# Optimization experiments

Hardware: AMD Instinct MI355X
Metric: run time of the kernel (lower is better)

Reference implementation:

```python
import jax, jax.numpy as jnp
import numpy as np

N_NODES = 50000
N_EDGES = 800000
IN_F, H_F, OUT_F = 256, 256, 128


def setup_inputs() -> dict:
    key = jax.random.key(0)
    k1, k2, k3, k4, k5, k6 = jax.random.split(key, 6)
    in_feat = jax.random.normal(k1, (N_NODES, IN_F), dtype=jnp.float32)
    src = jax.random.randint(k2, (N_EDGES,), 0, N_NODES, dtype=jnp.int32)
    dst = jax.random.randint(k3, (N_EDGES,), 0, N_NODES, dtype=jnp.int32)
    s1 = 1.0 / np.sqrt(IN_F)
    s2 = 1.0 / np.sqrt(H_F)
    W1 = jax.random.uniform(k4, (IN_F, H_F), dtype=jnp.float32, minval=-s1, maxval=s1)
    b1 = jnp.zeros((H_F,), dtype=jnp.float32)
    W2 = jax.random.uniform(k5, (H_F, OUT_F), dtype=jnp.float32, minval=-s2, maxval=s2)
    b2 = jnp.zeros((OUT_F,), dtype=jnp.float32)
    return {"in_feat": in_feat, "src": src, "dst": dst,
            "W1": W1, "b1": b1, "W2": W2, "b2": b2}


def _graph_conv(x, W, b, src, dst, n_nodes):
    # DGL GraphConv with norm='both':
    #   h = D_in^{-1/2} A D_out^{-1/2} (X W) + b   (degrees clamped to min 1)
    ones = jnp.ones((src.shape[0],), dtype=x.dtype)
    deg_out = jax.ops.segment_sum(ones, src, num_segments=n_nodes)
    deg_in = jax.ops.segment_sum(ones, dst, num_segments=n_nodes)
    norm_out = jax.lax.rsqrt(jnp.maximum(deg_out, 1.0))  # [N]
    norm_in = jax.lax.rsqrt(jnp.maximum(deg_in, 1.0))    # [N]
    h = (x @ W) * norm_out[:, None]                       # [N, F_out]
    agg = jax.ops.segment_sum(h[src], dst, num_segments=n_nodes)  # SpMM
    return agg * norm_in[:, None] + b


def reference(in_feat, src, dst, W1, b1, W2, b2):
    n = in_feat.shape[0]
    h = _graph_conv(in_feat, W1, b1, src, dst, n)
    h = jax.nn.relu(h)
    h = _graph_conv(h, W2, b2, src, dst, n)
    # dgl.mean_nodes over a single graph -> mean across all nodes
    return jnp.mean(h, axis=0)  # [OUT_F]
```

## Files before the change

### kernel.cpp

```cpp
#include <hip/hip_runtime.h>


#define NNODES 50000
#define NEDGES 800000
#define G1_BM   ((NNODES + 127) / 128)
#define MEGA_NB 3911
#define WS_NB   4096

typedef __bf16 bf16x8 __attribute__((ext_vector_type(8)));
typedef float f32x4 __attribute__((ext_vector_type(4)));
typedef float f32x2 __attribute__((ext_vector_type(2)));

__device__ __forceinline__ unsigned short f2b(float f) {
    union { float f; unsigned u; } v; v.f = f;
    unsigned r = 0x7fffu + ((v.u >> 16) & 1u);
    return (unsigned short)((v.u + r) >> 16);
}
__device__ __forceinline__ unsigned char f2fp8(float x) {
    return (unsigned char)(__builtin_amdgcn_cvt_pk_fp8_f32(x, x, 0, false) & 0xff);
}
__device__ __forceinline__ float rdeg(int d) {
    return __frsqrt_rn((float)max(d, 1));
}

__global__ void k_cast_w1(const float* __restrict__ W1, unsigned short* __restrict__ W1t) {
    int id = blockIdx.x * blockDim.x + threadIdx.x;
    int k = id >> 8, n = id & 255;
    W1t[n * 256 + k] = f2b(W1[id]);
}

__global__ __launch_bounds__(256) void k_mega1(
    const int* __restrict__ src, const int* __restrict__ dst,
    int* __restrict__ degOut, int* __restrict__ degIn,
    unsigned short* __restrict__ col2, unsigned short* __restrict__ dst2,
    const float* __restrict__ X, const unsigned short* __restrict__ W1t,
    unsigned char* __restrict__ H, int M) {
    __shared__ __align__(16) unsigned short As[128][40];
    __shared__ __align__(16) unsigned short Bs[128][40];

    int bid = blockIdx.x;
    int tid = threadIdx.x;

    if ((bid % 5) != 4) {
        int did = bid - (bid + 1) / 5;
        int e = did * 256 + tid;
        if (e < NEDGES) {
            int s = src[e], d = dst[e];
            int si = atomicAdd(&degIn[d], 1);
            if (si < 64) col2[d * 64 + si] = (unsigned short)s;
            int so = atomicAdd(&degOut[s], 1);
            if (so < 64) dst2[s * 64 + so] = (unsigned short)d;
        }
        return;
    }

    int g = bid / 5;
    int bm = g % G1_BM, bn = g / G1_BM;
    int m0 = bm * 128, n0 = bn * 128;
    int lane = tid & 63, wave = tid >> 6;
    int wm = (wave >> 1) * 64, wn = (wave & 1) * 64;
    int q = lane >> 4, r16 = lane & 15;

    f32x4 acc[4][4];
#pragma unroll
    for (int i = 0; i < 4; i++)
#pragma unroll
        for (int j = 0; j < 4; j++) acc[i][j] = 0.f;

    int c0 = tid, c1 = tid + 256;
    int r0 = c0 >> 2, k0c = (c0 & 3) * 8;
    int r1 = c1 >> 2, k1c = (c1 & 3) * 8;
    const float* Ar0 = X + (size_t)min(m0 + r0, M - 1) * 256;
    const float* Ar1 = X + (size_t)min(m0 + r1, M - 1) * 256;
    const unsigned short* Br0 = W1t + (size_t)(n0 + r0) * 256;
    const unsigned short* Br1 = W1t + (size_t)(n0 + r1) * 256;

    auto pk2u = [](float a, float b) -> unsigned {
        unsigned short x = f2b(a), y = f2b(b);
        return (unsigned)x | ((unsigned)y << 16);
    };

    for (int k0 = 0; k0 < 256; k0 += 32) {
        float4 fa0 = *(const float4*)(Ar0 + k0 + k0c);
        float4 fa1 = *(const float4*)(Ar0 + k0 + k0c + 4);
        float4 fb0 = *(const float4*)(Ar1 + k0 + k1c);
        float4 fb1 = *(const float4*)(Ar1 + k0 + k1c + 4);
        uint4 vb0 = *(const uint4*)(Br0 + k0 + k0c);
        uint4 vb1 = *(const uint4*)(Br1 + k0 + k1c);
        uint4 va0 = make_uint4(pk2u(fa0.x, fa0.y), pk2u(fa0.z, fa0.w), pk2u(fa1.x, fa1.y), pk2u(fa1.z, fa1.w));
        uint4 va1 = make_uint4(pk2u(fb0.x, fb0.y), pk2u(fb0.z, fb0.w), pk2u(fb1.x, fb1.y), pk2u(fb1.z, fb1.w));
        __syncthreads();
        *(uint4*)&As[r0][k0c] = va0;
        *(uint4*)&As[r1][k1c] = va1;
        *(uint4*)&Bs[r0][k0c] = vb0;
        *(uint4*)&Bs[r1][k1c] = vb1;
        __syncthreads();
        bf16x8 af[4], bf[4];
#pragma unroll
        for (int i = 0; i < 4; i++)
            af[i] = *(const bf16x8*)&As[wm + i * 16 + r16][q * 8];
#pragma unroll
        for (int j = 0; j < 4; j++)
            bf[j] = *(const bf16x8*)&Bs[wn + j * 16 + r16][q * 8];
#pragma unroll
        for (int i = 0; i < 4; i++)
#pragma unroll
            for (int j = 0; j < 4; j++)
                acc[i][j] = __builtin_amdgcn_mfma_f32_16x16x32_bf16(af[i], bf[j], acc[i][j], 0, 0, 0);
    }

#pragma unroll
    for (int i = 0; i < 4; i++) {
#pragma unroll
        for (int rr = 0; rr < 4; rr++) {
            int m = m0 + wm + i * 16 + q * 4 + rr;
            if (m < M) {
                unsigned char* Hp = H + (size_t)m * 256 + n0 + wn + r16;
#pragma unroll
                for (int j = 0; j < 4; j++)
                    Hp[j * 16] = f2fp8(acc[i][j][rr]);
            }
        }
    }
}

__global__ __launch_bounds__(256) void k_spmm_wsum(
    const unsigned char* __restrict__ H, const int* __restrict__ degIn,
    const int* __restrict__ degOut, const unsigned short* __restrict__ col2,
    const unsigned short* __restrict__ dst2, const float* __restrict__ bias,
    float* __restrict__ vpart) {
    __shared__ float sm[4][256];
    int wave = threadIdx.x >> 6;
    int lane = threadIdx.x & 63;
    int f = lane * 4;
    const unsigned char* Hf = H + f;
    float4 bv = *(const float4*)(bias + f);
    float vac0 = 0.f, vac1 = 0.f, vac2 = 0.f, vac3 = 0.f;

    for (int qd = blockIdx.x; qd < NNODES / 4; qd += gridDim.x) {
        int node = qd * 4 + wave;

        int dO = min(degOut[node], 64);
        float sIn = 0.f;
        if (lane < dO) sIn = rdeg(degIn[(int)dst2[node * 64 + lane]]);
#pragma unroll
        for (int o = 32; o > 0; o >>= 1) sIn += __shfl_xor(sIn, o);
        float wn = rdeg(dO) * sIn;

        int s = node * 64;
        int e = s + min(degIn[node], 64);
        float a0 = 0.f, a1 = 0.f, a2 = 0.f, a3 = 0.f;
        int i = s;
        for (; i + 8 <= e; i += 8) {
            int c[8];
#pragma unroll
            for (int u = 0; u < 8; u++) c[u] = __builtin_amdgcn_readfirstlane((int)col2[i + u]);
            float w[8]; unsigned v[8];
#pragma unroll
            for (int u = 0; u < 8; u++) {
                w[u] = rdeg(degOut[c[u]]);
                v[u] = *(const unsigned*)(Hf + (size_t)c[u] * 256);
            }
#pragma unroll
            for (int u = 0; u < 8; u++) {
                f32x2 lo = __builtin_amdgcn_cvt_pk_f32_fp8(v[u], false);
                f32x2 hi = __builtin_amdgcn_cvt_pk_f32_fp8(v[u], true);
                a0 += lo.x * w[u]; a1 += lo.y * w[u];
                a2 += hi.x * w[u]; a3 += hi.y * w[u];
            }
        }
        for (; i < e; i++) {
            int c = __builtin_amdgcn_readfirstlane((int)col2[i]);
            float w = rdeg(degOut[c]);
            unsigned v = *(const unsigned*)(Hf + (size_t)c * 256);
            f32x2 lo = __builtin_amdgcn_cvt_pk_f32_fp8(v, false);
            f32x2 hi = __builtin_amdgcn_cvt_pk_f32_fp8(v, true);
            a0 += lo.x * w; a1 += lo.y * w;
            a2 += hi.x * w; a3 += hi.y * w;
        }
        float nm = rdeg(e - s);
        vac0 += wn * fmaxf(a0 * nm + bv.x, 0.f);
        vac1 += wn * fmaxf(a1 * nm + bv.y, 0.f);
        vac2 += wn * fmaxf(a2 * nm + bv.z, 0.f);
        vac3 += wn * fmaxf(a3 * nm + bv.w, 0.f);
    }

    *(float4*)&sm[wave][f] = make_float4(vac0, vac1, vac2, vac3);
    __syncthreads();
    int t = threadIdx.x;
    float s4 = sm[0][t] + sm[1][t] + sm[2][t] + sm[3][t];
    vpart[(size_t)blockIdx.x * 256 + t] = s4;
}

__global__ __launch_bounds__(256) void k_red1(const float* __restrict__ vpart,
                                              float* __restrict__ vred) {
    int b = blockIdx.x;
    int t = threadIdx.x;
    float s = 0.f;
    for (int i = b; i < WS_NB; i += 64) s += vpart[(size_t)i * 256 + t];
    vred[(size_t)b * 256 + t] = s;
}

__global__ __launch_bounds__(1024) void k_final(
    const float* __restrict__ vred, const float* __restrict__ W2,
    const float* __restrict__ b2, float* __restrict__ out) {
    __shared__ float part[4][256];
    __shared__ float v[256];
    int t = threadIdx.x;
    int feat = t & 255, pr = t >> 8;
    float s = 0.f;
    for (int i = pr; i < 64; i += 4) s += vred[(size_t)i * 256 + feat];
    part[pr][feat] = s;
    __syncthreads();
    if (t < 256) v[t] = part[0][t] + part[1][t] + part[2][t] + part[3][t];
    __syncthreads();
    if (t < 128) {
        float o = 0.f;
        for (int k = 0; k < 256; k++) o += v[k] * W2[k * 128 + t];
        out[t] = o * (1.0f / (float)NNODES) + b2[t];
    }
}

extern "C" void kernel_launch(void* const* d_in, const int* in_sizes, int n_in,
                              void* d_out, int out_size, void* d_ws, size_t ws_size,
                              hipStream_t stream) {
    const float* X   = (const float*)d_in[0];
    const int*   src = (const int*)d_in[1];
    const int*   dst = (const int*)d_in[2];
    const float* W1  = (const float*)d_in[3];
    const float* b1  = (const float*)d_in[4];
    const float* W2  = (const float*)d_in[5];
    const float* b2  = (const float*)d_in[6];
    float* out = (float*)d_out;

    const int n = NNODES;

    char* p = (char*)d_ws;
    auto carve = [&](size_t bytes) -> void* {
        void* r = (void*)p;
        p += (bytes + 255) & ~(size_t)255;
        return r;
    };
    int*   degOut  = (int*)carve((size_t)2 * n * sizeof(int));
    int*   degIn   = degOut + n;
    unsigned short* col2 = (unsigned short*)carve((size_t)n * 64 * 2);
    unsigned short* dst2 = (unsigned short*)carve((size_t)n * 64 * 2);
    unsigned short* W1t  = (unsigned short*)carve((size_t)256 * 256 * 2);
    unsigned char*  bufA = (unsigned char*)carve((size_t)n * 256);
    float* vpart  = (float*)carve((size_t)WS_NB * 256 * sizeof(float));
    float* vred   = (float*)carve((size_t)64 * 256 * sizeof(float));

    hipMemsetAsync(degOut, 0, (size_t)2 * n * sizeof(int), stream);

    k_cast_w1<<<256, 256, 0, stream>>>(W1, W1t);

    k_mega1<<<MEGA_NB, 256, 0, stream>>>(src, dst, degOut, degIn, col2, dst2, X, W1t, bufA, n);

    k_spmm_wsum<<<WS_NB, 256, 0, stream>>>(bufA, degIn, degOut, col2, dst2, b1, vpart);

    k_red1<<<64, 256, 0, stream>>>(vpart, vred);
    k_final<<<1, 1024, 0, stream>>>(vred, W2, b2, out);
}
```

Before: 246.6 us.

## Pre-scale GEMM output by out-degree norm in a separate pass before SpMM

The GEMM now writes bf16 output, and a new k_scale pass multiplies each row by its out-degree norm and packs it to fp8. This removes the per-edge degOut gather and rsqrt from the SpMM inner loop. The memset is folded into the W1 cast kernel, and the edge blocks in the mega kernel now handle two edges per thread with 2:1 interleaving. The cost is an extra bf16 round trip of the full hidden matrix (about 25MB written and read) plus one more kernel launch.

```diff
diff --git a/kernel.cpp b/kernel.cpp
--- a/kernel.cpp
+++ b/kernel.cpp
@@ -4,7 +4,9 @@
 #define NNODES 50000
 #define NEDGES 800000
 #define G1_BM   ((NNODES + 127) / 128)
-#define MEGA_NB 3911
+#define G1_NB   (G1_BM * 2)
+#define EDGE_NB ((NEDGES + 511) / 512)
+#define MEGA_NB 2346
 #define WS_NB   4096
 
 typedef __bf16 bf16x8 __attribute__((ext_vector_type(8)));
@@ -16,17 +18,21 @@
     unsigned r = 0x7fffu + ((v.u >> 16) & 1u);
     return (unsigned short)((v.u + r) >> 16);
 }
-__device__ __forceinline__ unsigned char f2fp8(float x) {
-    return (unsigned char)(__builtin_amdgcn_cvt_pk_fp8_f32(x, x, 0, false) & 0xff);
+__device__ __forceinline__ float b2f(unsigned s) {
+    union { unsigned u; float f; } v; v.u = s << 16; return v.f;
 }
 __device__ __forceinline__ float rdeg(int d) {
     return __frsqrt_rn((float)max(d, 1));
 }
 
-__global__ void k_cast_w1(const float* __restrict__ W1, unsigned short* __restrict__ W1t) {
+__global__ void k_cast_zero(const float* __restrict__ W1, unsigned short* __restrict__ W1t,
+                            int* __restrict__ degs) {
     int id = blockIdx.x * blockDim.x + threadIdx.x;
-    int k = id >> 8, n = id & 255;
-    W1t[n * 256 + k] = f2b(W1[id]);
+    if (id < 65536) {
+        int k = id >> 8, n = id & 255;
+        W1t[n * 256 + k] = f2b(W1[id]);
+    }
+    if (id < 2 * NNODES) degs[id] = 0;
 }
 
 __global__ __launch_bounds__(256) void k_mega1(
@@ -34,18 +40,29 @@
     int* __restrict__ degOut, int* __restrict__ degIn,
     unsigned short* __restrict__ col2, unsigned short* __restrict__ dst2,
     const float* __restrict__ X, const unsigned short* __restrict__ W1t,
-    unsigned char* __restrict__ H, int M) {
+    unsigned short* __restrict__ Hb, int M) {
     __shared__ __align__(16) unsigned short As[128][40];
     __shared__ __align__(16) unsigned short Bs[128][40];
 
     int bid = blockIdx.x;
     int tid = threadIdx.x;
 
-    if ((bid % 5) != 4) {
-        int did = bid - (bid + 1) / 5;
-        int e = did * 256 + tid;
-        if (e < NEDGES) {
-            int s = src[e], d = dst[e];
+    if ((bid % 3) != 2) {
+        int did = (bid / 3) * 2 + (bid % 3);
+        int e0 = did * 512 + tid * 2;
+        if (e0 + 1 < NEDGES) {
+            int2 s2 = *(const int2*)(src + e0);
+            int2 d2 = *(const int2*)(dst + e0);
+            int si = atomicAdd(&degIn[d2.x], 1);
+            if (si < 64) col2[d2.x * 64 + si] = (unsigned short)s2.x;
+            int so = atomicAdd(&degOut[s2.x], 1);
+            if (so < 64) dst2[s2.x * 64 + so] = (unsigned short)d2.x;
+            si = atomicAdd(&degIn[d2.y], 1);
+            if (si < 64) col2[d2.y * 64 + si] = (unsigned short)s2.y;
+            so = atomicAdd(&degOut[s2.y], 1);
+            if (so < 64) dst2[s2.y * 64 + so] = (unsigned short)d2.y;
+        } else if (e0 < NEDGES) {
+            int s = src[e0], d = dst[e0];
             int si = atomicAdd(&degIn[d], 1);
             if (si < 64) col2[d * 64 + si] = (unsigned short)s;
             int so = atomicAdd(&degOut[s], 1);
@@ -54,7 +71,7 @@
         return;
     }
 
-    int g = bid / 5;
+    int g = bid / 3;
     int bm = g % G1_BM, bn = g / G1_BM;
     int m0 = bm * 128, n0 = bn * 128;
     int lane = tid & 63, wave = tid >> 6;
@@ -115,13 +132,29 @@
         for (int rr = 0; rr < 4; rr++) {
             int m = m0 + wm + i * 16 + q * 4 + rr;
             if (m < M) {
-                unsigned char* Hp = H + (size_t)m * 256 + n0 + wn + r16;
+                unsigned short* Hp = Hb + (size_t)m * 256 + n0 + wn + r16;
 #pragma unroll
                 for (int j = 0; j < 4; j++)
-                    Hp[j * 16] = f2fp8(acc[i][j][rr]);
+                    Hp[j * 16] = f2b(acc[i][j][rr]);
             }
         }
     }
+}
+
+__global__ __launch_bounds__(256) void k_scale(
+    const unsigned short* __restrict__ Hb, const int* __restrict__ degOut,
+    unsigned char* __restrict__ H) {
+    int wave = threadIdx.x >> 6;
+    int lane = threadIdx.x & 63;
+    int row = blockIdx.x * 4 + wave;
+    float s = rdeg(degOut[row]);
+    const unsigned short* hp = Hb + (size_t)row * 256 + lane * 4;
+    uint2 v = *(const uint2*)hp;
+    float f0 = b2f(v.x & 0xffff) * s, f1 = b2f(v.x >> 16) * s;
+    float f2 = b2f(v.y & 0xffff) * s, f3 = b2f(v.y >> 16) * s;
+    unsigned lo = __builtin_amdgcn_cvt_pk_fp8_f32(f0, f1, 0, false);
+    unsigned packed = __builtin_amdgcn_cvt_pk_fp8_f32(f2, f3, lo, true);
+    *(unsigned*)(H + (size_t)row * 256 + lane * 4) = packed;
 }
 
 __global__ __launch_bounds__(256) void k_spmm_wsum(
@@ -155,28 +188,22 @@
             int c[8];
 #pragma unroll
             for (int u = 0; u < 8; u++) c[u] = __builtin_amdgcn_readfirstlane((int)col2[i + u]);
-            float w[8]; unsigned v[8];
-#pragma unroll
-            for (int u = 0; u < 8; u++) {
-                w[u] = rdeg(degOut[c[u]]);
-                v[u] = *(const unsigned*)(Hf + (size_t)c[u] * 256);
-            }
+            unsigned v[8];
+#pragma unroll
+            for (int u = 0; u < 8; u++) v[u] = *(const unsigned*)(Hf + (size_t)c[u] * 256);
 #pragma unroll
             for (int u = 0; u < 8; u++) {
                 f32x2 lo = __builtin_amdgcn_cvt_pk_f32_fp8(v[u], false);
                 f32x2 hi = __builtin_amdgcn_cvt_pk_f32_fp8(v[u], true);
-                a0 += lo.x * w[u]; a1 += lo.y * w[u];
-                a2 += hi.x * w[u]; a3 += hi.y * w[u];
+                a0 += lo.x; a1 += lo.y; a2 += hi.x; a3 += hi.y;
             }
         }
         for (; i < e; i++) {
             int c = __builtin_amdgcn_readfirstlane((int)col2[i]);
-            float w = rdeg(degOut[c]);
             unsigned v = *(const unsigned*)(Hf + (size_t)c * 256);
             f32x2 lo = __builtin_amdgcn_cvt_pk_f32_fp8(v, false);
             f32x2 hi = __builtin_amdgcn_cvt_pk_f32_fp8(v, true);
-            a0 += lo.x * w; a1 += lo.y * w;
-            a2 += hi.x * w; a3 += hi.y * w;
+            a0 += lo.x; a1 += lo.y; a2 += hi.x; a3 += hi.y;
         }
         float nm = rdeg(e - s);
         vac0 += wn * fmaxf(a0 * nm + bv.x, 0.f);
@@ -246,17 +273,18 @@
     unsigned short* col2 = (unsigned short*)carve((size_t)n * 64 * 2);
     unsigned short* dst2 = (unsigned short*)carve((size_t)n * 64 * 2);
     unsigned short* W1t  = (unsigned short*)carve((size_t)256 * 256 * 2);
-    unsigned char*  bufA = (unsigned char*)carve((size_t)n * 256);
+    unsigned short* Hb   = (unsigned short*)carve((size_t)n * 256 * 2);
+    unsigned char*  Hs   = (unsigned char*)carve((size_t)n * 256);
     float* vpart  = (float*)carve((size_t)WS_NB * 256 * sizeof(float));
     float* vred   = (float*)carve((size_t)64 * 256 * sizeof(float));
 
-    hipMemsetAsync(degOut, 0, (size_t)2 * n * sizeof(int), stream);
-
-    k_cast_w1<<<256, 256, 0, stream>>>(W1, W1t);
-
-    k_mega1<<<MEGA_NB, 256, 0, stream>>>(src, dst, degOut, degIn, col2, dst2, X, W1t, bufA, n);
-
-    k_spmm_wsum<<<WS_NB, 256, 0, stream>>>(bufA, degIn, degOut, col2, dst2, b1, vpart);
+    k_cast_zero<<<392, 256, 0, stream>>>(W1, W1t, degOut);
+
+    k_mega1<<<MEGA_NB, 256, 0, stream>>>(src, dst, degOut, degIn, col2, dst2, X, W1t, Hb, n);
+
+    k_scale<<<n / 4, 256, 0, stream>>>(Hb, degOut, Hs);
+
+    k_spmm_wsum<<<WS_NB, 256, 0, stream>>>(Hs, degIn, degOut, col2, dst2, b1, vpart);
 
     k_red1<<<64, 256, 0, stream>>>(vpart, vred);
     k_final<<<1, 1024, 0, stream>>>(vred, W2, b2, out);
```

Result: slower. 253.3 us (+2.7%).
